# Performance work log

Measured on AMD Instinct MI355X. Metric: run time of the kernel, lower is better.

The kernel has to match this reference:

```python
import jax, jax.numpy as jnp
import numpy as np

B, T, FB, C = 2, 256, 128, 128
H_T, H_F, BAND = 4, 4, 16
INNER = 4 * C


def setup_inputs() -> dict:
    key = jax.random.key(0)
    ks = jax.random.split(key, 8)
    g = lambda k, shp: jax.random.normal(k, shp, jnp.float32) * 0.02
    return {
        "x": jax.random.normal(ks[0], (B, T, FB, C), jnp.float32),
        # temporal pre-norm + MHA (in_proj [3C,C], out_proj [C,C])
        "ln_t_w": jnp.ones((C,), jnp.float32), "ln_t_b": jnp.zeros((C,), jnp.float32),
        "t_wi": g(ks[1], (3 * C, C)), "t_bi": jnp.zeros((3 * C,), jnp.float32),
        "t_wo": g(ks[2], (C, C)), "t_bo": jnp.zeros((C,), jnp.float32),
        # frequency pre-norm + MHA
        "ln_f_w": jnp.ones((C,), jnp.float32), "ln_f_b": jnp.zeros((C,), jnp.float32),
        "f_wi": g(ks[3], (3 * C, C)), "f_bi": jnp.zeros((3 * C,), jnp.float32),
        "f_wo": g(ks[4], (C, C)), "f_bo": jnp.zeros((C,), jnp.float32),
        # FFN pre-norm + two linears
        "ln_n_w": jnp.ones((C,), jnp.float32), "ln_n_b": jnp.zeros((C,), jnp.float32),
        "w1": g(ks[5], (INNER, C)), "b1": jnp.zeros((INNER,), jnp.float32),
        "w2": g(ks[6], (C, INNER)), "b2": jnp.zeros((C,), jnp.float32),
    }


def _ln(x, w, b, eps=1e-5):
    mu = x.mean(-1, keepdims=True)
    var = ((x - mu) ** 2).mean(-1, keepdims=True)
    return (x - mu) * jax.lax.rsqrt(var + eps) * w + b


def _mha(x, wi, bi, wo, bo, h, mask):
    """torch.nn.MultiheadAttention equivalent. x: [..., S, C], mask: additive [S, S]."""
    c = x.shape[-1]
    dh = c // h
    qkv = x @ wi.T + bi
    q, k, v = jnp.split(qkv, 3, axis=-1)
    split = lambda t: t.reshape(t.shape[:-1] + (h, dh)).swapaxes(-2, -3)  # [..., h, S, dh]
    q, k, v = split(q), split(k), split(v)
    scores = jnp.einsum('...hqd,...hkd->...hqk', q, k) * (1.0 / np.sqrt(dh)) + mask
    attn = jax.nn.softmax(scores, axis=-1)
    o = jnp.einsum('...hqk,...hkd->...hqd', attn, v)
    o = o.swapaxes(-2, -3).reshape(x.shape)
    return o @ wo.T + bo


def _causal_mask(n):
    i = jnp.arange(n)
    return jnp.where(i[:, None] >= i[None, :], 0.0, -jnp.inf).astype(jnp.float32)


def _band_mask(n, band):
    i = jnp.arange(n)
    return jnp.where(jnp.abs(i[:, None] - i[None, :]) <= band, 0.0, -jnp.inf).astype(jnp.float32)


def reference(x, ln_t_w, ln_t_b, t_wi, t_bi, t_wo, t_bo,
              ln_f_w, ln_f_b, f_wi, f_bi, f_wo, f_bo,
              ln_n_w, ln_n_b, w1, b1, w2, b2):
    cm = _causal_mask(x.shape[1])      # [T, T]
    bm = _band_mask(x.shape[2], BAND)  # [F, F]
    # temporal causal MHSA per frequency bin (pre-norm residual)
    xt = _ln(x, ln_t_w, ln_t_b).transpose(0, 2, 1, 3)  # [B, F, T, C]
    x = x + _mha(xt, t_wi, t_bi, t_wo, t_bo, H_T, cm).transpose(0, 2, 1, 3)
    # banded local MHSA over frequency per time step
    xf = _ln(x, ln_f_w, ln_f_b)  # [B, T, F, C]
    x = x + _mha(xf, f_wi, f_bi, f_wo, f_bo, H_F, bm)
    # FFN (Linear -> exact GELU -> Linear)
    xn = _ln(x, ln_n_w, ln_n_b)
    h = jax.nn.gelu(xn @ w1.T + b1, approximate=False)
    x = x + (h @ w2.T + b2)
    return x
```

## Files before the change

kernel.cpp:

```cpp
#include <hip/hip_runtime.h>
#include <math.h>

typedef __bf16 bf16;
typedef __bf16 bf16x8 __attribute__((ext_vector_type(8)));
typedef __bf16 bf16x4 __attribute__((ext_vector_type(4)));
typedef __bf16 bf16x2 __attribute__((ext_vector_type(2)));
typedef float f32x4 __attribute__((ext_vector_type(4)));
typedef float f32x2 __attribute__((ext_vector_type(2)));
typedef float f32x16 __attribute__((ext_vector_type(16)));
typedef unsigned int u32;
typedef unsigned int u32x4 __attribute__((ext_vector_type(4)));

#define AS1 __attribute__((address_space(1)))
#define AS3 __attribute__((address_space(3)))

static __device__ __forceinline__ f32x4 mfma16(bf16x8 a, bf16x8 b, f32x4 c) {
    return __builtin_amdgcn_mfma_f32_16x16x32_bf16(a, b, c, 0, 0, 0);
}
static __device__ __forceinline__ f32x16 mfma32(bf16x8 a, bf16x8 b, f32x16 c) {
    return __builtin_amdgcn_mfma_f32_32x32x16_bf16(a, b, c, 0, 0, 0);
}
static __device__ __forceinline__ u32 pk2(float a, float b) {
    bf16x2 v; v[0] = (bf16)a; v[1] = (bf16)b;
    return __builtin_bit_cast(u32, v);
}
static __device__ __forceinline__ float gelu_f(float x) {
    float u = 0.7978845608f * x * __builtin_fmaf(0.044715f, x * x, 1.0f);
    float e = __expf(2.0f * u);
    return x - x * __builtin_amdgcn_rcpf(e + 1.0f);
}

__global__ __launch_bounds__(256) void cvt_w6(
    const float* __restrict__ s0, const float* __restrict__ s1,
    const float* __restrict__ s2, const float* __restrict__ s3,
    const float* __restrict__ s4, const float* __restrict__ s5,
    bf16* __restrict__ dst)
{
    int i = (blockIdx.x * 256 + threadIdx.x) * 4;
    const float* src; int off;
    if      (i <  49152) { src = s0; off = 0; }
    else if (i <  65536) { src = s1; off = 49152; }
    else if (i < 114688) { src = s2; off = 65536; }
    else if (i < 131072) { src = s3; off = 114688; }
    else if (i < 196608) { src = s4; off = 131072; }
    else                 { src = s5; off = 196608; }
    f32x4 v = *(const f32x4*)&src[i - off];
    bf16x4 b;
    b[0] = (bf16)v[0]; b[1] = (bf16)v[1]; b[2] = (bf16)v[2]; b[3] = (bf16)v[3];
    *(bf16x4*)&dst[i] = b;
}

template<int OUT_BF16, int RES, int RESBF, int GELU_, int LNA, int RMAP, int KT, int NT>
__global__ __launch_bounds__(256) void gemm_rw(
    const bf16* __restrict__ A, const bf16* __restrict__ W,
    const float* __restrict__ bias, const void* __restrict__ res,
    void* __restrict__ outp,
    const float* __restrict__ xf, const float* __restrict__ lnaw,
    const float* __restrict__ lnab)
{
    constexpr int N = NT * 128;
    __shared__ __align__(16) bf16 Bs[128 * 64];
    const int tid  = threadIdx.x;
    const int lane = tid & 63;
    const int w    = tid >> 6;
    const int li = lane & 15, g = lane >> 4;
    const int m0 = blockIdx.x * 64;
    const int arow = m0 + w * 16 + li;
    int srow = arow;
    if constexpr (RMAP) {
        int b = arow >> 15, t = (arow >> 7) & 255, f = arow & 127;
        srow = (b << 15) + (f << 8) + t;
    }
    const bf16* ap = A + (size_t)srow * KT;

    bf16x8 afrag[4];
    if constexpr (LNA) {
        int b = arow >> 15, f = (arow >> 8) & 127, t = arow & 255;
        const float* xp = xf + (((size_t)b * 256 + t) * 128 + f) * 128;
        f32x4 cv[8];
        #pragma unroll
        for (int cc = 0; cc < 4; ++cc) {
            cv[2 * cc]     = *(const f32x4*)&xp[cc * 32 + g * 8];
            cv[2 * cc + 1] = *(const f32x4*)&xp[cc * 32 + g * 8 + 4];
        }
        float sm = 0.f, sq = 0.f;
        #pragma unroll
        for (int i = 0; i < 8; ++i)
            #pragma unroll
            for (int j = 0; j < 4; ++j) { float v = cv[i][j]; sm += v; sq += v * v; }
        sm += __shfl_xor(sm, 16); sm += __shfl_xor(sm, 32);
        sq += __shfl_xor(sq, 16); sq += __shfl_xor(sq, 32);
        float mu = sm * 0.0078125f;
        float rs = rsqrtf(sq * 0.0078125f - mu * mu + 1e-5f);
        #pragma unroll
        for (int cc = 0; cc < 4; ++cc) {
            f32x4 w0 = *(const f32x4*)&lnaw[cc * 32 + g * 8];
            f32x4 w1 = *(const f32x4*)&lnaw[cc * 32 + g * 8 + 4];
            f32x4 b0 = *(const f32x4*)&lnab[cc * 32 + g * 8];
            f32x4 b1 = *(const f32x4*)&lnab[cc * 32 + g * 8 + 4];
            #pragma unroll
            for (int j = 0; j < 4; ++j) {
                afrag[cc][j]     = (bf16)((cv[2 * cc][j]     - mu) * rs * w0[j] + b0[j]);
                afrag[cc][4 + j] = (bf16)((cv[2 * cc + 1][j] - mu) * rs * w1[j] + b1[j]);
            }
        }
    } else if constexpr (KT == 128) {
        #pragma unroll
        for (int cc = 0; cc < 4; ++cc)
            afrag[cc] = *(const bf16x8*)&ap[cc * 32 + g * 8];
    }

    #pragma unroll
    for (int t = 0; t < NT; ++t) {
        const int n0 = t * 128;
        f32x4 acc[8] = {};

        #pragma unroll
        for (int k0 = 0; k0 < KT; k0 += 64) {
            #pragma unroll
            for (int it = 0; it < 4; ++it) {
                int idx = it * 256 + tid;
                int brow = idx >> 3, bch = idx & 7;
                const bf16* gp = W + (size_t)(n0 + brow) * KT + k0 + ((bch ^ (brow & 7)) * 8);
                __builtin_amdgcn_global_load_lds((AS1 void*)gp, (AS3 void*)(Bs + idx * 8), 16, 0, 0);
            }
            bf16x8 av0, av1;
            if constexpr (KT != 128) {
                av0 = *(const bf16x8*)&ap[k0 + g * 8];
                av1 = *(const bf16x8*)&ap[k0 + 32 + g * 8];
            }
            __syncthreads();
            #pragma unroll
            for (int kk = 0; kk < 2; ++kk) {
                bf16x8 av;
                if constexpr (KT == 128) av = afrag[(k0 >> 5) + kk];
                else                     av = kk ? av1 : av0;
                #pragma unroll
                for (int j = 0; j < 8; ++j) {
                    int brow = j * 16 + li;
                    int bch = (kk * 4 + g) ^ (li & 7);
                    bf16x8 bv = *(const bf16x8*)&Bs[brow * 64 + bch * 8];
                    acc[j] = mfma16(av, bv, acc[j]);
                }
            }
            __syncthreads();
        }

        float bcol[8];
        #pragma unroll
        for (int j = 0; j < 8; ++j) bcol[j] = bias[n0 + j * 16 + li];

        const int row0 = m0 + w * 16 + g * 4;
        #pragma unroll
        for (int r = 0; r < 4; ++r) {
            int row = row0 + r;
            #pragma unroll
            for (int j = 0; j < 8; ++j) {
                size_t off = (size_t)row * N + n0 + j * 16 + li;
                float v = acc[j][r] + bcol[j];
                if constexpr (RES) {
                    if constexpr (RESBF) v += (float)((const bf16*)res)[off];
                    else                 v += ((const float*)res)[off];
                }
                if constexpr (GELU_) v = gelu_f(v);
                if constexpr (OUT_BF16) ((bf16*)outp)[off] = (bf16)v;
                else                    ((float*)outp)[off] = v;
            }
        }
    }
}

template<int MODE, int RESBF>
__global__ __launch_bounds__(256) void attn_fused(
    const bf16* __restrict__ qkv, const bf16* __restrict__ Wo,
    const float* __restrict__ bo, const void* __restrict__ res,
    bf16* __restrict__ xc, bf16* __restrict__ xn,
    const float* __restrict__ lnw, const float* __restrict__ lnb)
{
    constexpr int S = (MODE == 0) ? 256 : 128;
    __shared__ __align__(16) char smem[2 * 20480 + 2048];
    float* red = (float*)(smem + 40960);
    const int tid = threadIdx.x;
    const int lane = tid & 63;
    const int w = tid >> 6;
    const int hi = lane >> 5;
    const int q31 = lane & 31;
    const int s = blockIdx.x;
    const int qb = blockIdx.y * 64;

    const size_t base = (size_t)s * S * 384;
    const bf16* qp = qkv + base + w * 32;

    const float sc = 0.17677669529663687f;
    bf16x8 qA0, qA1, qB0, qB1;
    {
        bf16x8 r0 = *(const bf16x8*)&qp[(size_t)(qb + q31) * 384 + hi * 8];
        bf16x8 r1 = *(const bf16x8*)&qp[(size_t)(qb + q31) * 384 + 16 + hi * 8];
        bf16x8 r2 = *(const bf16x8*)&qp[(size_t)(qb + 32 + q31) * 384 + hi * 8];
        bf16x8 r3 = *(const bf16x8*)&qp[(size_t)(qb + 32 + q31) * 384 + 16 + hi * 8];
        #pragma unroll
        for (int e = 0; e < 8; ++e) {
            qA0[e] = (bf16)((float)r0[e] * sc);
            qA1[e] = (bf16)((float)r1[e] * sc);
            qB0[e] = (bf16)((float)r2[e] * sc);
            qB1[e] = (bf16)((float)r3[e] * sc);
        }
    }

    f32x16 OA = {}, OB = {};
    float lA = 0.f, lB = 0.f;

    int klo, khi;
    if constexpr (MODE == 0) { klo = 0; khi = qb + 64; }
    else {
        klo = (qb > 16 ? (qb - 16) : 0) & ~31;
        khi = (qb + 80 < S) ? (qb + 80) : S;
    }

    const int seg = tid & 15, rw = tid >> 4;
    const char* qc = (const char*)qkv + base * 2;
    const int wdst = (seg >> 2) * 2560 + rw * 80 + (seg & 3) * 16;

    u32x4 rk0, rk1, rv0, rv1;
    auto gload = [&](int k0) {
        const char* r0 = qc + (size_t)(k0 + rw) * 768;
        const char* r1 = qc + (size_t)(k0 + rw + 16) * 768;
        rk0 = *(const u32x4*)(r0 + 256 + seg * 16);
        rk1 = *(const u32x4*)(r1 + 256 + seg * 16);
        rv0 = *(const u32x4*)(r0 + 512 + seg * 16);
        rv1 = *(const u32x4*)(r1 + 512 + seg * 16);
    };
    auto swrite = [&](char* buf) {
        *(u32x4*)(buf + wdst)                = rk0;
        *(u32x4*)(buf + wdst + 1280)         = rk1;
        *(u32x4*)(buf + 10240 + wdst)        = rv0;
        *(u32x4*)(buf + 10240 + wdst + 1280) = rv1;
    };

    gload(klo);
    swrite(smem);
    __syncthreads();
    int cur = 0;

    for (int k0 = klo; k0 < khi; k0 += 32) {
        bool notlast = (k0 + 32 < khi);
        if (notlast) gload(k0 + 32);

        char* buf = smem + cur * 20480;
        const char* kb = buf + w * 2560 + q31 * 80 + hi * 16;
        bf16x8 kf0 = *(const bf16x8*)(kb);
        bf16x8 kf1 = *(const bf16x8*)(kb + 32);
        const bf16* vb = (const bf16*)(buf + 10240) + w * 1280 + hi * 320 + q31;
        bf16x8 vf1, vf2;
        #pragma unroll
        for (int e = 0; e < 8; ++e) {
            vf1[e] = vb[e * 40];
            vf2[e] = vb[640 + e * 40];
        }

        auto step = [&](f32x16& O, float& l, bf16x8 q0, bf16x8 q1,
                        int qrow, bool doMask) {
            f32x16 st = {};
            st = mfma32(kf0, q0, st);
            st = mfma32(kf1, q1, st);
            if (doMask) {
                #pragma unroll
                for (int r = 0; r < 16; ++r) {
                    int krow = k0 + (r & 3) + 8 * (r >> 2) + 4 * hi;
                    bool ok;
                    if constexpr (MODE == 0) ok = (krow <= qrow);
                    else { int d = krow - qrow; ok = (d <= 16 && d >= -16); }
                    st[r] = ok ? st[r] : -3.0e38f;
                }
            }
            float ps = 0.f;
            #pragma unroll
            for (int r = 0; r < 16; ++r) {
                float p = __expf(st[r]);
                st[r] = p;
                ps += p;
            }
            ps += __shfl_xor(ps, 32);
            l += ps;

            u32 c01 = pk2(st[0], st[1]),   c23 = pk2(st[2], st[3]);
            u32 c45 = pk2(st[4], st[5]),   c67 = pk2(st[6], st[7]);
            u32 c89 = pk2(st[8], st[9]),   cAB = pk2(st[10], st[11]);
            u32 cCD = pk2(st[12], st[13]), cEF = pk2(st[14], st[15]);
            u32 x01 = __shfl_xor((int)c01, 32), x23 = __shfl_xor((int)c23, 32);
            u32 x45 = __shfl_xor((int)c45, 32), x67 = __shfl_xor((int)c67, 32);
            u32 x89 = __shfl_xor((int)c89, 32), xAB = __shfl_xor((int)cAB, 32);
            u32 xCD = __shfl_xor((int)cCD, 32), xEF = __shfl_xor((int)cEF, 32);
            u32x4 b1w = hi ? u32x4{x45, x67, c45, c67} : u32x4{c01, c23, x01, x23};
            u32x4 b2w = hi ? u32x4{xCD, xEF, cCD, cEF} : u32x4{c89, cAB, x89, xAB};
            bf16x8 B1 = __builtin_bit_cast(bf16x8, b1w);
            bf16x8 B2 = __builtin_bit_cast(bf16x8, b2w);

            O = mfma32(vf1, B1, O);
            O = mfma32(vf2, B2, O);
        };

        bool actA, actB, dgA, dgB;
        if constexpr (MODE == 0) {
            actA = (k0 <= qb); actB = true;
            dgA = (k0 == qb);  dgB = (k0 == qb + 32);
        } else {
            actA = (k0 >= qb - 47) && (k0 <= qb + 47);
            actB = (k0 >= qb - 15) && (k0 <= qb + 79);
            dgA = true; dgB = true;
        }
        if (actA) step(OA, lA, qA0, qA1, qb + q31, dgA);
        if (actB) step(OB, lB, qB0, qB1, qb + 32 + q31, dgB);

        if (notlast) swrite(smem + (cur ^ 1) * 20480);
        __syncthreads();
        cur ^= 1;
    }

    bf16* o_lds = (bf16*)smem;
    float invA = 1.f / lA, invB = 1.f / lB;
    #pragma unroll
    for (int mb = 0; mb < 4; ++mb) {
        bf16x4 ovA, ovB;
        #pragma unroll
        for (int j = 0; j < 4; ++j) {
            ovA[j] = (bf16)(OA[mb * 4 + j] * invA);
            ovB[j] = (bf16)(OB[mb * 4 + j] * invB);
        }
        *(bf16x4*)&o_lds[q31 * 136 + w * 32 + mb * 8 + hi * 4] = ovA;
        *(bf16x4*)&o_lds[(32 + q31) * 136 + w * 32 + mb * 8 + hi * 4] = ovB;
    }
    __syncthreads();

    const int li = lane & 15, g = lane >> 4;
    bf16x8 af[4][4];
    #pragma unroll
    for (int mi = 0; mi < 4; ++mi)
        #pragma unroll
        for (int kk = 0; kk < 4; ++kk)
            af[mi][kk] = *(const bf16x8*)&o_lds[(mi * 16 + li) * 136 + kk * 32 + g * 8];

    f32x4 acc[4][2] = {};
    #pragma unroll
    for (int ni = 0; ni < 2; ++ni) {
        #pragma unroll
        for (int kk = 0; kk < 4; ++kk) {
            bf16x8 bv = *(const bf16x8*)&Wo[(size_t)(w * 32 + ni * 16 + li) * 128 + kk * 32 + g * 8];
            #pragma unroll
            for (int mi = 0; mi < 4; ++mi)
                acc[mi][ni] = mfma16(af[mi][kk], bv, acc[mi][ni]);
        }
    }

    float vals[4][2][4];
    #pragma unroll
    for (int mi = 0; mi < 4; ++mi) {
        #pragma unroll
        for (int r = 0; r < 4; ++r) {
            int lrl = mi * 16 + g * 4 + r;
            int grow = qb + lrl;
            size_t rrow;
            if constexpr (MODE == 0) {
                int b = s >> 7, f = s & 127;
                rrow = ((size_t)(b * 256 + grow)) * 128 + f;
            } else {
                int b = s >> 8, t = s & 255;
                rrow = (size_t)b * 32768 + (size_t)grow * 256 + t;
            }
            #pragma unroll
            for (int ni = 0; ni < 2; ++ni) {
                int col = w * 32 + ni * 16 + li;
                float v = acc[mi][ni][r] + bo[col];
                if constexpr (RESBF) v += (float)((const bf16*)res)[rrow * 128 + col];
                else                 v += ((const float*)res)[rrow * 128 + col];
                vals[mi][ni][r] = v;
            }
        }
    }
    #pragma unroll
    for (int mi = 0; mi < 4; ++mi) {
        #pragma unroll
        for (int r = 0; r < 4; ++r) {
            float sm = vals[mi][0][r] + vals[mi][1][r];
            float sq = vals[mi][0][r] * vals[mi][0][r] + vals[mi][1][r] * vals[mi][1][r];
            #pragma unroll
            for (int off = 1; off < 16; off <<= 1) {
                sm += __shfl_xor(sm, off);
                sq += __shfl_xor(sq, off);
            }
            if (li == 0) {
                red[(mi * 16 + g * 4 + r) * 8 + w * 2 + 0] = sm;
                red[(mi * 16 + g * 4 + r) * 8 + w * 2 + 1] = sq;
            }
        }
    }
    __syncthreads();
    #pragma unroll
    for (int mi = 0; mi < 4; ++mi) {
        #pragma unroll
        for (int r = 0; r < 4; ++r) {
            int mrow = mi * 16 + g * 4 + r;
            f32x4 p0 = *(const f32x4*)&red[mrow * 8 + 0];
            f32x4 p1 = *(const f32x4*)&red[mrow * 8 + 4];
            float smt = p0[0] + p0[2] + p1[0] + p1[2];
            float sqt = p0[1] + p0[3] + p1[1] + p1[3];
            float mu = smt * 0.0078125f;
            float rs = rsqrtf(sqt * 0.0078125f - mu * mu + 1e-5f);
            size_t woff = ((size_t)s * S + qb + mrow) * 128;
            #pragma unroll
            for (int ni = 0; ni < 2; ++ni) {
                int col = w * 32 + ni * 16 + li;
                float v = vals[mi][ni][r];
                xc[woff + col] = (bf16)v;
                xn[woff + col] = (bf16)((v - mu) * rs * lnw[col] + lnb[col]);
            }
        }
    }
}

extern "C" void kernel_launch(void* const* d_in, const int* in_sizes, int n_in,
                              void* d_out, int out_size, void* d_ws, size_t ws_size,
                              hipStream_t stream) {
    const float* x      = (const float*)d_in[0];
    const float* ln_t_w = (const float*)d_in[1];
    const float* ln_t_b = (const float*)d_in[2];
    const float* t_wi   = (const float*)d_in[3];
    const float* t_bi   = (const float*)d_in[4];
    const float* t_wo   = (const float*)d_in[5];
    const float* t_bo   = (const float*)d_in[6];
    const float* ln_f_w = (const float*)d_in[7];
    const float* ln_f_b = (const float*)d_in[8];
    const float* f_wi   = (const float*)d_in[9];
    const float* f_bi   = (const float*)d_in[10];
    const float* f_wo   = (const float*)d_in[11];
    const float* f_bo   = (const float*)d_in[12];
    const float* ln_n_w = (const float*)d_in[13];
    const float* ln_n_b = (const float*)d_in[14];
    const float* w1     = (const float*)d_in[15];
    const float* b1     = (const float*)d_in[16];
    const float* w2     = (const float*)d_in[17];
    const float* b2     = (const float*)d_in[18];

    char* ws = (char*)d_ws;
    bf16* wbf  = (bf16*)ws;
    bf16* xn   = (bf16*)(ws + 524288);
    bf16* qkvh = (bf16*)(ws + 524288 + 16777216);
    bf16* xcA  = (bf16*)(ws + 524288 + 16777216 + 67108864 + 16777216);
    bf16* xcB  = (bf16*)(ws + 524288 + 16777216 + 67108864 + 2 * 16777216);
    float* out = (float*)d_out;

    const bf16* twi_b = wbf + 0;
    const bf16* two_b = wbf + 49152;
    const bf16* fwi_b = wbf + 65536;
    const bf16* fwo_b = wbf + 114688;
    const bf16* w1_b  = wbf + 131072;
    const bf16* w2_b  = wbf + 196608;

    cvt_w6<<<256, 256, 0, stream>>>(t_wi, t_wo, f_wi, f_wo, w1, w2, wbf);

    gemm_rw<1, 0, 0, 0, 1, 0, 128, 3><<<1024, 256, 0, stream>>>(
        nullptr, twi_b, t_bi, nullptr, qkvh, x, ln_t_w, ln_t_b);
    attn_fused<0, 0><<<dim3(256, 4), 256, 0, stream>>>(
        qkvh, two_b, t_bo, x, xcA, xn, ln_f_w, ln_f_b);

    gemm_rw<1, 0, 0, 0, 0, 1, 128, 3><<<1024, 256, 0, stream>>>(
        xn, fwi_b, f_bi, nullptr, qkvh, nullptr, nullptr, nullptr);
    attn_fused<1, 1><<<dim3(512, 2), 256, 0, stream>>>(
        qkvh, fwo_b, f_bo, xcA, xcB, xn, ln_n_w, ln_n_b);

    gemm_rw<1, 0, 0, 1, 0, 0, 128, 4><<<1024, 256, 0, stream>>>(
        xn, w1_b, b1, nullptr, qkvh, nullptr, nullptr, nullptr);
    gemm_rw<0, 1, 1, 0, 0, 0, 512, 1><<<1024, 256, 0, stream>>>(
        qkvh, w2_b, b2, xcB, out, nullptr, nullptr, nullptr);

    (void)in_sizes; (void)n_in; (void)out_size; (void)ws_size;
}
```

Baseline: 161.6 us.

## Fuse FFN up-projection, GELU and down-projection into one kernel

Replaces the two separate FFN GEMM launches with a single kernel. Each 64-row tile computes the 512-wide hidden activation in 128-column chunks, applies bias and GELU, stages the chunk as bf16 in LDS, and immediately accumulates it into the down-projection output. This removes the global write and re-read of the hidden tensor and one kernel launch. The cost is that W1 and W2 tiles are reloaded per block with little overlap, and the chain of serialized syncs may limit occupancy.

```diff
diff --git a/kernel.cpp b/kernel.cpp
--- a/kernel.cpp
+++ b/kernel.cpp
@@ -166,6 +166,126 @@
                 if constexpr (OUT_BF16) ((bf16*)outp)[off] = (bf16)v;
                 else                    ((float*)outp)[off] = v;
             }
+        }
+    }
+}
+
+__global__ __launch_bounds__(256) void ffn_fused(
+    const bf16* __restrict__ A, const bf16* __restrict__ W1,
+    const float* __restrict__ b1, const bf16* __restrict__ W2,
+    const float* __restrict__ b2, const bf16* __restrict__ res,
+    float* __restrict__ outp)
+{
+    __shared__ __align__(16) bf16 Bs[128 * 64];
+    __shared__ __align__(16) bf16 hbuf[64 * 136];
+    const int tid  = threadIdx.x;
+    const int lane = tid & 63;
+    const int w    = tid >> 6;
+    const int li = lane & 15, g = lane >> 4;
+    const int m0 = blockIdx.x * 64;
+    const int arow = m0 + w * 16 + li;
+    const bf16* ap = A + (size_t)arow * 128;
+
+    bf16x8 axn[4];
+    #pragma unroll
+    for (int cc = 0; cc < 4; ++cc)
+        axn[cc] = *(const bf16x8*)&ap[cc * 32 + g * 8];
+
+    const int sidx_brow = tid >> 1;
+
+    f32x4 oacc[8] = {};
+
+    #pragma unroll
+    for (int t = 0; t < 4; ++t) {
+        f32x4 hacc[8] = {};
+        #pragma unroll
+        for (int k0 = 0; k0 < 128; k0 += 64) {
+            #pragma unroll
+            for (int it = 0; it < 4; ++it) {
+                int idx = it * 256 + tid;
+                int brow = idx >> 3, bch = idx & 7;
+                const bf16* gp = W1 + (size_t)(t * 128 + brow) * 128 + k0 + ((bch ^ (brow & 7)) * 8);
+                __builtin_amdgcn_global_load_lds((AS1 void*)gp, (AS3 void*)(Bs + idx * 8), 16, 0, 0);
+            }
+            __syncthreads();
+            #pragma unroll
+            for (int kk = 0; kk < 2; ++kk) {
+                bf16x8 av = axn[(k0 >> 5) + kk];
+                #pragma unroll
+                for (int j = 0; j < 8; ++j) {
+                    int brow = j * 16 + li;
+                    int bch = (kk * 4 + g) ^ (li & 7);
+                    bf16x8 bv = *(const bf16x8*)&Bs[brow * 64 + bch * 8];
+                    hacc[j] = mfma16(av, bv, hacc[j]);
+                }
+            }
+            __syncthreads();
+        }
+
+        #pragma unroll
+        for (int it = 0; it < 4; ++it) {
+            int idx = it * 256 + tid;
+            int brow = idx >> 3, bch = idx & 7;
+            const bf16* gp = W2 + (size_t)brow * 512 + t * 128 + ((bch ^ (brow & 7)) * 8);
+            __builtin_amdgcn_global_load_lds((AS1 void*)gp, (AS3 void*)(Bs + idx * 8), 16, 0, 0);
+        }
+
+        float b1c[8];
+        #pragma unroll
+        for (int j = 0; j < 8; ++j) b1c[j] = b1[t * 128 + j * 16 + li];
+        #pragma unroll
+        for (int r = 0; r < 4; ++r) {
+            int lrow = w * 16 + g * 4 + r;
+            #pragma unroll
+            for (int j = 0; j < 8; ++j)
+                hbuf[lrow * 136 + j * 16 + li] = (bf16)gelu_f(hacc[j][r] + b1c[j]);
+        }
+        __syncthreads();
+
+        bf16x8 ah[4];
+        #pragma unroll
+        for (int cc = 0; cc < 4; ++cc)
+            ah[cc] = *(const bf16x8*)&hbuf[(w * 16 + li) * 136 + cc * 32 + g * 8];
+
+        #pragma unroll
+        for (int k0 = 0; k0 < 128; k0 += 64) {
+            if (k0) {
+                #pragma unroll
+                for (int it = 0; it < 4; ++it) {
+                    int idx = it * 256 + tid;
+                    int brow = idx >> 3, bch = idx & 7;
+                    const bf16* gp = W2 + (size_t)brow * 512 + t * 128 + k0 + ((bch ^ (brow & 7)) * 8);
+                    __builtin_amdgcn_global_load_lds((AS1 void*)gp, (AS3 void*)(Bs + idx * 8), 16, 0, 0);
+                }
+                __syncthreads();
+            }
+            #pragma unroll
+            for (int kk = 0; kk < 2; ++kk) {
+                bf16x8 av = ah[(k0 >> 5) + kk];
+                #pragma unroll
+                for (int j = 0; j < 8; ++j) {
+                    int brow = j * 16 + li;
+                    int bch = (kk * 4 + g) ^ (li & 7);
+                    bf16x8 bv = *(const bf16x8*)&Bs[brow * 64 + bch * 8];
+                    oacc[j] = mfma16(av, bv, oacc[j]);
+                }
+            }
+            __syncthreads();
+        }
+    }
+
+    float b2c[8];
+    #pragma unroll
+    for (int j = 0; j < 8; ++j) b2c[j] = b2[j * 16 + li];
+    const int row0 = m0 + w * 16 + g * 4;
+    #pragma unroll
+    for (int r = 0; r < 4; ++r) {
+        int row = row0 + r;
+        #pragma unroll
+        for (int j = 0; j < 8; ++j) {
+            size_t off = (size_t)row * 128 + j * 16 + li;
+            float v = oacc[j][r] + b2c[j] + (float)res[off];
+            outp[off] = v;
         }
     }
 }
@@ -468,10 +588,7 @@
     attn_fused<1, 1><<<dim3(512, 2), 256, 0, stream>>>(
         qkvh, fwo_b, f_bo, xcA, xcB, xn, ln_n_w, ln_n_b);
 
-    gemm_rw<1, 0, 0, 1, 0, 0, 128, 4><<<1024, 256, 0, stream>>>(
-        xn, w1_b, b1, nullptr, qkvh, nullptr, nullptr, nullptr);
-    gemm_rw<0, 1, 1, 0, 0, 0, 512, 1><<<1024, 256, 0, stream>>>(
-        qkvh, w2_b, b2, xcB, out, nullptr, nullptr, nullptr);
+    ffn_fused<<<1024, 256, 0, stream>>>(xn, w1_b, b1, w2_b, b2, xcB, out);
 
     (void)in_sizes; (void)n_in; (void)out_size; (void)ws_size;
 }
```

After: 154.2 us. 4.6% less time.
